# Performance work log

Measured on AMD Instinct MI355X. Metric: run time of the kernel, lower is better.

The kernel has to match this reference:

```python
import jax, jax.numpy as jnp
import numpy as np

N_NODES = 100000
HIDDEN = 128
N_EDGES = 1000000


def setup_inputs() -> dict:
    key = jax.random.key(0)
    k1, k2, k3 = jax.random.split(key, 3)
    z = jax.random.normal(k1, (N_NODES, HIDDEN), dtype=jnp.float32)
    edge_index = jax.random.randint(k2, (2, N_EDGES), 0, N_NODES, dtype=jnp.int64)
    # xavier_uniform for square matrix: bound = sqrt(6/(fan_in+fan_out))
    bound = float(np.sqrt(6.0 / (HIDDEN + HIDDEN)))
    weights = jax.random.uniform(k3, (HIDDEN, HIDDEN), dtype=jnp.float32,
                                 minval=-bound, maxval=bound)
    return {"z": z, "edge_index": edge_index, "weights": weights}


def reference(z, edge_index, weights):
    # symm=True: symmetrize the bilinear form
    W = weights + weights.T                      # [d, d]
    z_src = z[edge_index[0]]                     # [E, d] gather
    z_dst = z[edge_index[1]]                     # [E, d] gather
    # torch: (W @ z_dst.T).T == z_dst @ W.T
    value = jnp.einsum('ed,dk,ek->e', z_src, W, z_dst)  # row-wise bilinear score
    return jax.nn.sigmoid(value)
```

## Files before the change

### kernel.cpp

```cpp
#include <hip/hip_runtime.h>

#define HIDDEN 128
#define LDSW 136
#define BSHIFT 10
#define NBMAX 128
#define CAP 10752
#define OVF_MAX 65536

typedef _Float16 f16;
typedef f16 f16x2 __attribute__((ext_vector_type(2)));
typedef f16 f16x8 __attribute__((ext_vector_type(8)));
typedef float f32x16 __attribute__((ext_vector_type(16)));
typedef unsigned long long ull;
typedef ull ull2 __attribute__((ext_vector_type(2)));

static __device__ __forceinline__ float fdot2(f16x2 a, f16x2 b, float c) {
    return __builtin_amdgcn_fdot2(a, b, c, false);
}

__global__ __launch_bounds__(256) void prep_w(const float* __restrict__ w,
                                              f16* __restrict__ wsh_t,
                                              int* __restrict__ cursor,
                                              int* __restrict__ ovf_cnt) {
    int idx = blockIdx.x * 256 + threadIdx.x;
    if (idx < NBMAX) cursor[idx] = idx * CAP;
    if (idx == NBMAX) ovf_cnt[0] = 0;
    int n = idx >> 7, k = idx & 127;
    wsh_t[idx] = (f16)(w[k * HIDDEN + n] + w[n * HIDDEN + k]);
}

__global__ __launch_bounds__(256) void gemm_scatter(const float* __restrict__ z,
                                                    const f16* __restrict__ wsh_t,
                                                    f16* __restrict__ zh,
                                                    f16* __restrict__ uh,
                                                    const int* __restrict__ eidx,
                                                    int* __restrict__ cursor,
                                                    ull* __restrict__ perm,
                                                    ull* __restrict__ ovf,
                                                    int* __restrict__ ovf_cnt,
                                                    int nrows, int E, int nb, int ngemm) {
    __shared__ f16 wlt[HIDDEN * LDSW];
    int tid = threadIdx.x;

    if (blockIdx.x >= ngemm) {
        int* lh    = (int*)wlt;
        int* lbase = lh + NBMAX;
        int* lrank = lbase + NBMAX;
        int base = (blockIdx.x - ngemm) * 4096;
        if (tid < NBMAX) { lh[tid] = 0; lrank[tid] = 0; }
        __syncthreads();
        int s[16], d[16], bb[16];
        #pragma unroll
        for (int i = 0; i < 16; ++i) {
            int e = base + i * 256 + tid;
            bb[i] = -1;
            if (e < E) {
                s[i] = eidx[e]; d[i] = eidx[E + e];
                bb[i] = d[i] >> BSHIFT;
                atomicAdd(&lh[bb[i]], 1);
            }
        }
        __syncthreads();
        if (tid < nb && lh[tid]) lbase[tid] = atomicAdd(&cursor[tid], lh[tid]);
        __syncthreads();
        #pragma unroll
        for (int i = 0; i < 16; ++i) {
            if (bb[i] >= 0) {
                int e = base + i * 256 + tid;
                int r = atomicAdd(&lrank[bb[i]], 1);
                long pos = (long)lbase[bb[i]] + r;
                ull v = (ull)s[i] | ((ull)d[i] << 17) | ((ull)(e + 1) << 34);
                if (pos < (long)(bb[i] + 1) * CAP) perm[pos] = v;
                else {
                    int o = atomicAdd(ovf_cnt, 1);
                    if (o < OVF_MAX) ovf[o] = v;
                }
            }
        }
        return;
    }

    {
        const f16x8* g = (const f16x8*)wsh_t;
        #pragma unroll
        for (int it = 0; it < 8; ++it) {
            int idx = it * 256 + tid;
            int j = idx >> 4, kc = idx & 15;
            *(f16x8*)&wlt[j * LDSW + kc * 8] = g[idx];
        }
    }
    __syncthreads();

    int wave = tid >> 6, lane = tid & 63;
    int row0 = blockIdx.x * 128 + wave * 32;
    if (row0 > nrows - 32) row0 = nrows - 32;

    int m = lane & 31, half = lane >> 5;
    const float* zr = z  + (size_t)(row0 + m) * HIDDEN + half * 8;
    f16*        zhr = zh + (size_t)(row0 + m) * HIDDEN + half * 8;
    const f16* wbase = &wlt[m * LDSW + half * 8];

    f32x16 acc0, acc1, acc2, acc3;
    #pragma unroll
    for (int r = 0; r < 16; ++r) { acc0[r] = 0.f; acc1[r] = 0.f; acc2[r] = 0.f; acc3[r] = 0.f; }

    #pragma unroll
    for (int ks = 0; ks < 8; ++ks) {
        float4 a0 = *(const float4*)(zr + 16 * ks);
        float4 a1 = *(const float4*)(zr + 16 * ks + 4);
        f16x8 af = {(f16)a0.x, (f16)a0.y, (f16)a0.z, (f16)a0.w,
                    (f16)a1.x, (f16)a1.y, (f16)a1.z, (f16)a1.w};
        *(f16x8*)(zhr + 16 * ks) = af;
        f16x8 b0 = *(const f16x8*)(wbase + 16 * ks);
        f16x8 b1 = *(const f16x8*)(wbase + 32 * LDSW + 16 * ks);
        f16x8 b2 = *(const f16x8*)(wbase + 64 * LDSW + 16 * ks);
        f16x8 b3 = *(const f16x8*)(wbase + 96 * LDSW + 16 * ks);
        acc0 = __builtin_amdgcn_mfma_f32_32x32x16_f16(af, b0, acc0, 0, 0, 0);
        acc1 = __builtin_amdgcn_mfma_f32_32x32x16_f16(af, b1, acc1, 0, 0, 0);
        acc2 = __builtin_amdgcn_mfma_f32_32x32x16_f16(af, b2, acc2, 0, 0, 0);
        acc3 = __builtin_amdgcn_mfma_f32_32x32x16_f16(af, b3, acc3, 0, 0, 0);
    }

    f16* ur = uh + (size_t)row0 * HIDDEN;
    #pragma unroll
    for (int r = 0; r < 16; ++r) {
        int row = (r & 3) + 8 * (r >> 2) + 4 * half;
        f16* p = ur + (size_t)row * HIDDEN + m;
        p[0]  = (f16)acc0[r];
        p[32] = (f16)acc1[r];
        p[64] = (f16)acc2[r];
        p[96] = (f16)acc3[r];
    }
}

static __device__ __forceinline__ void score_edge(const f16* uh, const f16* zh,
                                                  ull p, float* out, int t, int E) {
    int src = (int)(p & 0x1FFFF);
    int dst = (int)((p >> 17) & 0x1FFFF);
    int ep  = (int)(p >> 34);
    const float4* a4 = (const float4*)(uh + (size_t)src * HIDDEN);
    const float4* b4 = (const float4*)(zh + (size_t)dst * HIDDEN);
    float4 av = a4[t], bv = b4[t];
    const f16x2* ap = (const f16x2*)&av;
    const f16x2* bp = (const f16x2*)&bv;
    float s = 0.f;
    #pragma unroll
    for (int i = 0; i < 4; ++i) s = fdot2(ap[i], bp[i], s);
    #pragma unroll
    for (int off = 8; off > 0; off >>= 1) s += __shfl_down(s, off, 16);
    if (t == 0 && ep > 0 && ep <= E) out[ep - 1] = 1.0f / (1.0f + __expf(-s));
}

__global__ __launch_bounds__(256, 8) void edge_bin(const f16* __restrict__ uh,
                                                   const f16* __restrict__ zh,
                                                   const ull* __restrict__ perm,
                                                   const ull* __restrict__ ovf,
                                                   const int* __restrict__ ovf_cnt,
                                                   float* __restrict__ out,
                                                   int E, int cpx, int nmain) {
    int tid = threadIdx.x;
    int g = tid >> 4, t = tid & 15;
    int b = blockIdx.x;
    if (b >= nmain) {
        int n = ovf_cnt[0];
        if (n > OVF_MAX) n = OVF_MAX;
        for (int i = (b - nmain) * 16 + g; i < n; i += 32 * 16)
            score_edge(uh, zh, ovf[i], out, t, E);
        return;
    }
    int chunk = (b & 7) * cpx + (b >> 3);
    long slot = (long)chunk * 32 + g * 2;
    ull2 p = *(const ull2*)&perm[slot];

    int src0 = (int)(p.x & 0x1FFFF), dst0 = (int)((p.x >> 17) & 0x1FFFF), e0 = (int)(p.x >> 34);
    int src1 = (int)(p.y & 0x1FFFF), dst1 = (int)((p.y >> 17) & 0x1FFFF), e1 = (int)(p.y >> 34);

    float4 a0 = ((const float4*)(uh + (size_t)src0 * HIDDEN))[t];
    float4 b0 = ((const float4*)(zh + (size_t)dst0 * HIDDEN))[t];
    float4 a1 = ((const float4*)(uh + (size_t)src1 * HIDDEN))[t];
    float4 b1 = ((const float4*)(zh + (size_t)dst1 * HIDDEN))[t];

    const f16x2* ap0 = (const f16x2*)&a0; const f16x2* bp0 = (const f16x2*)&b0;
    const f16x2* ap1 = (const f16x2*)&a1; const f16x2* bp1 = (const f16x2*)&b1;
    float s0 = 0.f, s1 = 0.f;
    #pragma unroll
    for (int i = 0; i < 4; ++i) {
        s0 = fdot2(ap0[i], bp0[i], s0);
        s1 = fdot2(ap1[i], bp1[i], s1);
    }
    #pragma unroll
    for (int off = 8; off > 0; off >>= 1) {
        s0 += __shfl_xor(s0, off, 16);
        s1 += __shfl_xor(s1, off, 16);
    }
    float sv = (t == 0) ? s0 : s1;
    int   ev = (t == 0) ? e0 : e1;
    if (t < 2 && ev > 0 && ev <= E) out[ev - 1] = 1.0f / (1.0f + __expf(-sv));
}

__global__ __launch_bounds__(256) void edge_score16(const f16* __restrict__ uh,
                                                    const f16* __restrict__ zh,
                                                    const int* __restrict__ eidx,
                                                    float* __restrict__ out, int E) {
    int tid = threadIdx.x;
    int g = tid >> 4, t = tid & 15;
    int e = blockIdx.x * 16 + g;
    if (e >= E) return;
    ull p = (ull)eidx[e] | ((ull)eidx[E + e] << 17) | ((ull)(e + 1) << 34);
    score_edge(uh, zh, p, out, t, E);
}

extern "C" void kernel_launch(void* const* d_in, const int* in_sizes, int n_in,
                              void* d_out, int out_size, void* d_ws, size_t ws_size,
                              hipStream_t stream) {
    const float* z    = (const float*)d_in[0];
    const int*   eidx = (const int*)d_in[1];
    const float* w    = (const float*)d_in[2];
    float* out = (float*)d_out;

    int nrows = in_sizes[0] / HIDDEN;
    int E = out_size;
    int nb = (nrows >> BSHIFT) + 1;

    f16* wsh_t  = (f16*)d_ws;
    f16* zh     = wsh_t + HIDDEN * HIDDEN;
    f16* uh     = zh + (size_t)nrows * HIDDEN;
    int* cursor = (int*)(uh + (size_t)nrows * HIDDEN);
    int* ovf_cnt = cursor + NBMAX;
    ull* ovf    = (ull*)(ovf_cnt + 4);
    ull* perm   = ovf + OVF_MAX;

    long nslots = (long)nb * CAP;
    size_t need = (size_t)((char*)(perm + nslots) - (char*)d_ws);
    bool binned = ws_size >= need;

    int ngemm = (nrows + 127) / 128;
    int nscat = (E + 4095) / 4096;

    prep_w<<<64, 256, 0, stream>>>(w, wsh_t, cursor, ovf_cnt);
    if (binned) {
        gemm_scatter<<<ngemm + nscat, 256, 0, stream>>>(z, wsh_t, zh, uh, eidx, cursor,
                                                        perm, ovf, ovf_cnt, nrows, E, nb, ngemm);
        long ngrp = nslots / 32;
        int cpx = (int)(ngrp / 8);
        int nmain = (int)ngrp;
        edge_bin<<<nmain + 32, 256, 0, stream>>>(uh, zh, perm, ovf, ovf_cnt, out, E, cpx, nmain);
    } else {
        gemm_scatter<<<ngemm, 256, 0, stream>>>(z, wsh_t, zh, uh, eidx, cursor,
                                                perm, ovf, ovf_cnt, nrows, E, nb, ngemm);
        edge_score16<<<(E + 15) / 16, 256, 0, stream>>>(uh, zh, eidx, out, E);
    }
}
```

Before: 158.4 us.

## Fuse weight symmetrization into GEMM blocks, swizzle LDS, reorder scatter blocks first

Drops the separate prep_w kernel. Each GEMM block now builds the symmetrized f16 weight tile straight into LDS from fp32 w, using an XOR swizzle in place of padding, and the bin cursors are reset with a memset. Scatter blocks are moved to the front of the grid so they are dispatched before the GEMM tiles, and bin positions become bin-relative. The aim is to save one launch and reorder work. The cost is that every GEMM block repeats the weight symmetrization with strided column reads.

```diff
diff --git a/kernel.cpp b/kernel.cpp
--- a/kernel.cpp
+++ b/kernel.cpp
@@ -1,7 +1,6 @@
 #include <hip/hip_runtime.h>
 
 #define HIDDEN 128
-#define LDSW 136
 #define BSHIFT 10
 #define NBMAX 128
 #define CAP 10752
@@ -9,6 +8,7 @@
 
 typedef _Float16 f16;
 typedef f16 f16x2 __attribute__((ext_vector_type(2)));
+typedef f16 f16x4 __attribute__((ext_vector_type(4)));
 typedef f16 f16x8 __attribute__((ext_vector_type(8)));
 typedef float f32x16 __attribute__((ext_vector_type(16)));
 typedef unsigned long long ull;
@@ -18,19 +18,8 @@
     return __builtin_amdgcn_fdot2(a, b, c, false);
 }
 
-__global__ __launch_bounds__(256) void prep_w(const float* __restrict__ w,
-                                              f16* __restrict__ wsh_t,
-                                              int* __restrict__ cursor,
-                                              int* __restrict__ ovf_cnt) {
-    int idx = blockIdx.x * 256 + threadIdx.x;
-    if (idx < NBMAX) cursor[idx] = idx * CAP;
-    if (idx == NBMAX) ovf_cnt[0] = 0;
-    int n = idx >> 7, k = idx & 127;
-    wsh_t[idx] = (f16)(w[k * HIDDEN + n] + w[n * HIDDEN + k]);
-}
-
 __global__ __launch_bounds__(256) void gemm_scatter(const float* __restrict__ z,
-                                                    const f16* __restrict__ wsh_t,
+                                                    const float* __restrict__ w,
                                                     f16* __restrict__ zh,
                                                     f16* __restrict__ uh,
                                                     const int* __restrict__ eidx,
@@ -38,15 +27,15 @@
                                                     ull* __restrict__ perm,
                                                     ull* __restrict__ ovf,
                                                     int* __restrict__ ovf_cnt,
-                                                    int nrows, int E, int nb, int ngemm) {
-    __shared__ f16 wlt[HIDDEN * LDSW];
+                                                    int nrows, int E, int nb, int nscat) {
+    __shared__ f16 wlt[HIDDEN * HIDDEN];
     int tid = threadIdx.x;
 
-    if (blockIdx.x >= ngemm) {
+    if (blockIdx.x < nscat) {
         int* lh    = (int*)wlt;
         int* lbase = lh + NBMAX;
         int* lrank = lbase + NBMAX;
-        int base = (blockIdx.x - ngemm) * 4096;
+        int base = blockIdx.x * 4096;
         if (tid < NBMAX) { lh[tid] = 0; lrank[tid] = 0; }
         __syncthreads();
         int s[16], d[16], bb[16];
@@ -68,9 +57,9 @@
             if (bb[i] >= 0) {
                 int e = base + i * 256 + tid;
                 int r = atomicAdd(&lrank[bb[i]], 1);
-                long pos = (long)lbase[bb[i]] + r;
+                int pib = lbase[bb[i]] + r;
                 ull v = (ull)s[i] | ((ull)d[i] << 17) | ((ull)(e + 1) << 34);
-                if (pos < (long)(bb[i] + 1) * CAP) perm[pos] = v;
+                if (pib < CAP) perm[(long)bb[i] * CAP + pib] = v;
                 else {
                     int o = atomicAdd(ovf_cnt, 1);
                     if (o < OVF_MAX) ovf[o] = v;
@@ -81,24 +70,31 @@
     }
 
     {
-        const f16x8* g = (const f16x8*)wsh_t;
         #pragma unroll
-        for (int it = 0; it < 8; ++it) {
-            int idx = it * 256 + tid;
-            int j = idx >> 4, kc = idx & 15;
-            *(f16x8*)&wlt[j * LDSW + kc * 8] = g[idx];
+        for (int it = 0; it < 16; ++it) {
+            int idx4 = (it * 256 + tid) * 4;
+            int n = idx4 >> 7, k0 = idx4 & 127;
+            float4 wr = *(const float4*)&w[n * HIDDEN + k0];
+            float c0 = w[(k0 + 0) * HIDDEN + n];
+            float c1 = w[(k0 + 1) * HIDDEN + n];
+            float c2 = w[(k0 + 2) * HIDDEN + n];
+            float c3 = w[(k0 + 3) * HIDDEN + n];
+            f16x4 v = {(f16)(wr.x + c0), (f16)(wr.y + c1), (f16)(wr.z + c2), (f16)(wr.w + c3)};
+            *(f16x4*)&wlt[n * HIDDEN + (k0 ^ ((n & 7) << 3))] = v;
         }
     }
     __syncthreads();
 
     int wave = tid >> 6, lane = tid & 63;
-    int row0 = blockIdx.x * 128 + wave * 32;
+    int tile = blockIdx.x - nscat;
+    int row0 = tile * 128 + wave * 32;
     if (row0 > nrows - 32) row0 = nrows - 32;
 
     int m = lane & 31, half = lane >> 5;
+    int swz = (m & 7) << 3;
     const float* zr = z  + (size_t)(row0 + m) * HIDDEN + half * 8;
     f16*        zhr = zh + (size_t)(row0 + m) * HIDDEN + half * 8;
-    const f16* wbase = &wlt[m * LDSW + half * 8];
+    const f16* wrow = &wlt[m * HIDDEN];
 
     f32x16 acc0, acc1, acc2, acc3;
     #pragma unroll
@@ -111,10 +107,11 @@
         f16x8 af = {(f16)a0.x, (f16)a0.y, (f16)a0.z, (f16)a0.w,
                     (f16)a1.x, (f16)a1.y, (f16)a1.z, (f16)a1.w};
         *(f16x8*)(zhr + 16 * ks) = af;
-        f16x8 b0 = *(const f16x8*)(wbase + 16 * ks);
-        f16x8 b1 = *(const f16x8*)(wbase + 32 * LDSW + 16 * ks);
-        f16x8 b2 = *(const f16x8*)(wbase + 64 * LDSW + 16 * ks);
-        f16x8 b3 = *(const f16x8*)(wbase + 96 * LDSW + 16 * ks);
+        int c = (half * 8 + 16 * ks) ^ swz;
+        f16x8 b0 = *(const f16x8*)&wrow[c];
+        f16x8 b1 = *(const f16x8*)&wrow[32 * HIDDEN + c];
+        f16x8 b2 = *(const f16x8*)&wrow[64 * HIDDEN + c];
+        f16x8 b3 = *(const f16x8*)&wrow[96 * HIDDEN + c];
         acc0 = __builtin_amdgcn_mfma_f32_32x32x16_f16(af, b0, acc0, 0, 0, 0);
         acc1 = __builtin_amdgcn_mfma_f32_32x32x16_f16(af, b1, acc1, 0, 0, 0);
         acc2 = __builtin_amdgcn_mfma_f32_32x32x16_f16(af, b2, acc2, 0, 0, 0);
@@ -222,8 +219,7 @@
     int E = out_size;
     int nb = (nrows >> BSHIFT) + 1;
 
-    f16* wsh_t  = (f16*)d_ws;
-    f16* zh     = wsh_t + HIDDEN * HIDDEN;
+    f16* zh     = (f16*)d_ws;
     f16* uh     = zh + (size_t)nrows * HIDDEN;
     int* cursor = (int*)(uh + (size_t)nrows * HIDDEN);
     int* ovf_cnt = cursor + NBMAX;
@@ -237,17 +233,18 @@
     int ngemm = (nrows + 127) / 128;
     int nscat = (E + 4095) / 4096;
 
-    prep_w<<<64, 256, 0, stream>>>(w, wsh_t, cursor, ovf_cnt);
+    hipMemsetAsync(cursor, 0, (NBMAX + 4) * sizeof(int), stream);
+
     if (binned) {
-        gemm_scatter<<<ngemm + nscat, 256, 0, stream>>>(z, wsh_t, zh, uh, eidx, cursor,
-                                                        perm, ovf, ovf_cnt, nrows, E, nb, ngemm);
+        gemm_scatter<<<nscat + ngemm, 256, 0, stream>>>(z, w, zh, uh, eidx, cursor,
+                                                        perm, ovf, ovf_cnt, nrows, E, nb, nscat);
         long ngrp = nslots / 32;
         int cpx = (int)(ngrp / 8);
         int nmain = (int)ngrp;
         edge_bin<<<nmain + 32, 256, 0, stream>>>(uh, zh, perm, ovf, ovf_cnt, out, E, cpx, nmain);
     } else {
-        gemm_scatter<<<ngemm, 256, 0, stream>>>(z, wsh_t, zh, uh, eidx, cursor,
-                                                perm, ovf, ovf_cnt, nrows, E, nb, ngemm);
+        gemm_scatter<<<ngemm, 256, 0, stream>>>(z, w, zh, uh, eidx, cursor,
+                                                perm, ovf, ovf_cnt, nrows, E, nb, 0);
         edge_score16<<<(E + 15) / 16, 256, 0, stream>>>(uh, zh, eidx, out, E);
     }
 }
```

Result: slower. 192.0 us (+21.2%).
